# Kernel optimization log

Hardware: AMD Instinct MI355X
Metric: run time of the kernel (lower is better)

Reference implementation:

```python
import jax, jax.numpy as jnp
import numpy as np

B, T, V = 8, 64, 25
IN_DIM = 64
HID = 64
D = 3 * HID // 2          # 96, per-node feature dim
OUT = 128
N = B * T * V * 2         # 25600 nodes
E = N * 16                # 409600 edges
LAYERS = 2
EPS = 1e-5


def prelu(x, a):
    return jnp.where(x >= 0, x, a * x)


def grouped_conv1x1(x, w, b, groups=3):
    # x: [B, C, V, T]; w: [O, C//groups]; b: [O]  (1x1 conv, groups=3)
    Bb, C, Vv, Tt = x.shape
    O = w.shape[0]
    xg = x.reshape(Bb, groups, C // groups, Vv, Tt)
    wg = w.reshape(groups, O // groups, C // groups)
    y = jnp.einsum('bgivt,goi->bgovt', xg, wg).reshape(Bb, O, Vv, Tt)
    return y + b[None, :, None, None]


def layer_norm(x, g, b):
    m = jnp.mean(x, axis=-1, keepdims=True)
    v = jnp.mean((x - m) ** 2, axis=-1, keepdims=True)
    return (x - m) / jnp.sqrt(v + EPS) * g + b


def _forward(h, src, dst, tp_w1, tp_b1, tp_a, tp_w2, tp_b2,
             tm_w1, tm_b1, tm_a, tm_w2, tm_b2,
             ln_g, ln_b, bn_g, bn_b, bn_rm, bn_rv, act_a,
             gW1, gb1, ga, gW2, gb2, t2_w, t2_b):
    # posture / motion streams -> [B, 3*in_dim, V, T]
    hp = jnp.transpose(h[:, :, :, 0, :], (0, 3, 2, 1))
    hm = jnp.transpose(h[:, :, :, 1, :], (0, 3, 2, 1))
    hp = grouped_conv1x1(prelu(grouped_conv1x1(hp, tp_w1, tp_b1), tp_a), tp_w2, tp_b2)
    hm = grouped_conv1x1(prelu(grouped_conv1x1(hm, tm_w1, tm_b1), tm_a), tm_w2, tm_b2)
    hp = jnp.transpose(hp, (0, 3, 2, 1))[:, :, :, None, :]  # [B,T,V,1,D]
    hm = jnp.transpose(hm, (0, 3, 2, 1))[:, :, :, None, :]
    x = jnp.concatenate([hp, hm], axis=3).reshape(-1, D)     # [N, D]
    raw = x
    hs, es = [], []
    for i in range(LAYERS):
        def gate(h2, i=i):
            # edge gate MLP: Linear -> PReLU -> Linear -> Tanh (dropout eval = id)
            return jnp.tanh(prelu(h2 @ gW1[i] + gb1[i], ga[i]) @ gW2[i] + gb2[i])
        e = gate(x[dst] * x[src])                            # [E, 1]
        z = jax.ops.segment_sum(x[src] * e, dst, num_segments=N)
        y = layer_norm(z + x, ln_g[i], ln_b[i])
        y = (y - bn_rm[i]) / jnp.sqrt(bn_rv[i] + EPS) * bn_g[i] + bn_b[i]  # BN eval
        x = prelu(y, act_a[i])
        hs.append(x)
        es.append(gate(x[dst] * x[src]))   # torch calls the layer a 2nd time for e
    hcat = jnp.concatenate([raw] + hs, axis=1)               # [N, 3D]
    out = hcat @ t2_w + t2_b                                 # dropout eval = id
    ee = jnp.concatenate(es, axis=0)                         # [2E, 1]
    return out, ee


def setup_inputs() -> dict:
    key = jax.random.key(0)
    ks = jax.random.split(key, 40)
    def nrm(k, shape, s=0.05):
        return jax.random.normal(k, shape, jnp.float32) * s
    d = {}
    d['h'] = jax.random.normal(ks[0], (B, T, V, 2, 3 * IN_DIM), jnp.float32)
    d['src'] = jax.random.randint(ks[1], (E,), 0, N, jnp.int32)
    d['dst'] = jax.random.randint(ks[2], (E,), 0, N, jnp.int32)
    # t1_posture / t1_motion grouped 1x1 convs
    d['tp_w1'] = nrm(ks[3], (3 * HID, IN_DIM)); d['tp_b1'] = nrm(ks[4], (3 * HID,))
    d['tp_a'] = jnp.full((1,), 0.25, jnp.float32)
    d['tp_w2'] = nrm(ks[5], (D, HID)); d['tp_b2'] = nrm(ks[6], (D,))
    d['tm_w1'] = nrm(ks[7], (3 * HID, IN_DIM)); d['tm_b1'] = nrm(ks[8], (3 * HID,))
    d['tm_a'] = jnp.full((1,), 0.25, jnp.float32)
    d['tm_w2'] = nrm(ks[9], (D, HID)); d['tm_b2'] = nrm(ks[10], (D,))
    # per-layer norms / activations (stacked over LAYERS)
    d['ln_g'] = jnp.ones((LAYERS, D), jnp.float32); d['ln_b'] = jnp.zeros((LAYERS, D), jnp.float32)
    d['bn_g'] = jnp.ones((LAYERS, D), jnp.float32); d['bn_b'] = jnp.zeros((LAYERS, D), jnp.float32)
    d['bn_rm'] = jnp.zeros((LAYERS, D), jnp.float32); d['bn_rv'] = jnp.ones((LAYERS, D), jnp.float32)
    d['act_a'] = jnp.full((LAYERS,), 0.25, jnp.float32)
    # per-layer FALayer gate MLP
    d['gW1'] = nrm(ks[11], (LAYERS, D, D)); d['gb1'] = nrm(ks[12], (LAYERS, D))
    d['ga'] = jnp.full((LAYERS,), 0.25, jnp.float32)
    d['gW2'] = nrm(ks[13], (LAYERS, D, 1)); d['gb2'] = nrm(ks[14], (LAYERS, 1))
    d['t2_w'] = nrm(ks[15], (3 * D, OUT)); d['t2_b'] = nrm(ks[16], (OUT,))
    return d


def reference(h, src, dst, tp_w1, tp_b1, tp_a, tp_w2, tp_b2,
              tm_w1, tm_b1, tm_a, tm_w2, tm_b2,
              ln_g, ln_b, bn_g, bn_b, bn_rm, bn_rv, act_a,
              gW1, gb1, ga, gW2, gb2, t2_w, t2_b):
    return _forward(h, src, dst, tp_w1, tp_b1, tp_a, tp_w2, tp_b2,
                    tm_w1, tm_b1, tm_a, tm_w2, tm_b2,
                    ln_g, ln_b, bn_g, bn_b, bn_rm, bn_rv, act_a,
                    gW1, gb1, ga, gW2, gb2, t2_w, t2_b)
```

## Files before the change

kernel.cpp:

```cpp
#include <hip/hip_runtime.h>

#define N_NODES 25600
#define N_EDGES 409600
#define EPSV 1e-5f

__device__ __forceinline__ unsigned short f2bf(float f) {
    unsigned int x = __float_as_uint(f);
    x += 0x7fffu + ((x >> 16) & 1u);
    return (unsigned short)(x >> 16);
}
__device__ __forceinline__ unsigned int f2bf2(float a, float b) {
#if __has_builtin(__builtin_amdgcn_cvt_pk_bf16_f32)
    auto r = __builtin_amdgcn_cvt_pk_bf16_f32(a, b);
    unsigned int u;
    __builtin_memcpy(&u, &r, 4);
    return u;
#else
    return (unsigned int)f2bf(a) | ((unsigned int)f2bf(b) << 16);
#endif
}

using frag_ab = __attribute__((ext_vector_type(8))) short;
using frag_cd = __attribute__((ext_vector_type(4))) float;
typedef _Float16 f16x8 __attribute__((ext_vector_type(8)));

#define TWST 72
#define THST 200

__global__ __launch_bounds__(256) void transform_mfma(
    const float* __restrict__ h,
    const float* __restrict__ tpw1, const float* __restrict__ tpb1, const float* __restrict__ tpa,
    const float* __restrict__ tpw2, const float* __restrict__ tpb2,
    const float* __restrict__ tmw1, const float* __restrict__ tmb1, const float* __restrict__ tma,
    const float* __restrict__ tmw2, const float* __restrict__ tmb2,
    float* __restrict__ xout, _Float16* __restrict__ xh)
{
    __shared__ alignas(16) unsigned short W1s[192 * TWST];
    __shared__ alignas(16) unsigned short W2s[96 * TWST];
    __shared__ alignas(16) unsigned short hs[64 * THST];
    __shared__ float b1s[192];
    __shared__ float b2s[96];

    const int tid = threadIdx.x;
    const int s = blockIdx.y;
    const float* w1 = s ? tmw1 : tpw1;
    const float* b1 = s ? tmb1 : tpb1;
    const float* w2 = s ? tmw2 : tpw2;
    const float* b2 = s ? tmb2 : tpb2;
    const float alpha = (s ? tma : tpa)[0];

    #pragma unroll
    for (int r = 0; r < 12; r++) {
        int idx4 = r * 256 + tid;
        int o = idx4 >> 4, i4 = (idx4 & 15) * 4;
        const float4 a = *(const float4*)&w1[o * 64 + i4];
        *(uint2*)&W1s[o * TWST + i4] = make_uint2(f2bf2(a.x, a.y), f2bf2(a.z, a.w));
    }
    #pragma unroll
    for (int r = 0; r < 6; r++) {
        int idx4 = r * 256 + tid;
        int o = idx4 >> 4, i4 = (idx4 & 15) * 4;
        const float4 a = *(const float4*)&w2[o * 64 + i4];
        *(uint2*)&W2s[o * TWST + i4] = make_uint2(f2bf2(a.x, a.y), f2bf2(a.z, a.w));
    }
    if (tid < 192) b1s[tid] = b1[tid];
    if (tid < 96) b2s[tid] = b2[tid];
    __syncthreads();

    const int lane = tid & 63;
    const int wv = tid >> 6;
    const int quad = lane >> 4;
    const int lcol = lane & 15;
    const int m0 = wv * 16;
    const int j0 = blockIdx.x * 64;

    #pragma unroll
    for (int r = 0; r < 12; r++) {
        int idx = r * 256 + tid;
        int m = idx / 48, q = idx - m * 48;
        const float4 a = *(const float4*)&h[(2 * (j0 + m) + s) * 192 + q * 4];
        *(uint2*)&hs[m * THST + q * 4] = make_uint2(f2bf2(a.x, a.y), f2bf2(a.z, a.w));
    }
    __syncthreads();

    const int arow = (m0 + lcol) * THST;
    #pragma unroll
    for (int g = 0; g < 3; g++) {
        frag_cd acc[4];
        #pragma unroll
        for (int nt = 0; nt < 4; nt++) acc[nt] = (frag_cd){0.f, 0.f, 0.f, 0.f};
        #pragma unroll
        for (int kt = 0; kt < 2; kt++) {
            const int k0 = kt * 32 + quad * 8;
            frag_ab af = *(const frag_ab*)&hs[arow + g * 64 + k0];
            #pragma unroll
            for (int nt = 0; nt < 4; nt++) {
                frag_ab bf = *(const frag_ab*)&W1s[(g * 64 + nt * 16 + lcol) * TWST + k0];
                acc[nt] = __builtin_amdgcn_mfma_f32_16x16x32_bf16(af, bf, acc[nt], 0, 0, 0);
            }
        }
        #pragma unroll
        for (int nt = 0; nt < 4; nt++) {
            const int o = g * 64 + nt * 16 + lcol;
            const float bv = b1s[o];
            #pragma unroll
            for (int reg = 0; reg < 4; reg++) {
                float u = acc[nt][reg] + bv;
                u = u >= 0.f ? u : alpha * u;
                hs[(m0 + quad * 4 + reg) * THST + o] = f2bf(u);
            }
        }
    }
    #pragma unroll
    for (int g2 = 0; g2 < 3; g2++) {
        frag_cd acc[2];
        acc[0] = (frag_cd){0.f, 0.f, 0.f, 0.f};
        acc[1] = (frag_cd){0.f, 0.f, 0.f, 0.f};
        #pragma unroll
        for (int kt = 0; kt < 2; kt++) {
            const int k0 = kt * 32 + quad * 8;
            frag_ab af = *(const frag_ab*)&hs[arow + g2 * 64 + k0];
            #pragma unroll
            for (int nt = 0; nt < 2; nt++) {
                frag_ab bf = *(const frag_ab*)&W2s[(g2 * 32 + nt * 16 + lcol) * TWST + k0];
                acc[nt] = __builtin_amdgcn_mfma_f32_16x16x32_bf16(af, bf, acc[nt], 0, 0, 0);
            }
        }
        #pragma unroll
        for (int nt = 0; nt < 2; nt++) {
            const int o2 = g2 * 32 + nt * 16 + lcol;
            const float bv = b2s[o2];
            #pragma unroll
            for (int reg = 0; reg < 4; reg++) {
                const int node = 2 * (j0 + m0 + quad * 4 + reg) + s;
                const float v = acc[nt][reg] + bv;
                xout[node * 96 + o2] = v;
                xh[node * 96 + o2] = (_Float16)v;
            }
        }
    }
}

template<bool DUAL>
__global__ __launch_bounds__(256) void gate_kernel(
    const _Float16* __restrict__ xh,
    const int* __restrict__ srcp, const int* __restrict__ dstp,
    const int* __restrict__ mapA,
    const float* __restrict__ gW1, const float* __restrict__ gb1,
    const float* __restrict__ ga,  const float* __restrict__ gW2,
    const float* __restrict__ gb2, int layerA, int layerB,
    float* __restrict__ outA, float* __restrict__ outB)
{
    __shared__ alignas(16) _Float16 W1f[(DUAL ? 2 : 1) * 9216];

    const int tid = threadIdx.x;
    {
        const float* W1p = gW1 + layerA * 9216;
        const float* W1q = gW1 + layerB * 9216;
        for (int fi = tid; fi < 1152; fi += 256) {
            int lc = fi & 15, r = fi >> 4;
            int quad = r & 3, t3 = r >> 2;
            int nt = t3 / 3, kt = t3 - nt * 3;
            int n = nt * 16 + lc, k0 = kt * 32 + quad * 8;
            f16x8 v, w;
            #pragma unroll
            for (int j = 0; j < 8; j++) {
                v[j] = (_Float16)W1p[(k0 + j) * 96 + n];
                if (DUAL) w[j] = (_Float16)W1q[(k0 + j) * 96 + n];
            }
            *(f16x8*)&W1f[fi * 8] = v;
            if (DUAL) *(f16x8*)&W1f[9216 + fi * 8] = w;
        }
    }

    const int lane = tid & 63;
    const int wv   = tid >> 6;
    const int quad = lane >> 4;
    const int lcol = lane & 15;
    const int m0   = wv * 16;
    const int erow = m0 + lcol;
    const int koff = quad * 8;

    float w2A[6], b1A[6], w2B[6], b1B[6];
    #pragma unroll
    for (int nt = 0; nt < 6; nt++) {
        w2A[nt] = gW2[layerA * 96 + nt * 16 + lcol];
        b1A[nt] = gb1[layerA * 96 + nt * 16 + lcol];
        if (DUAL) {
            w2B[nt] = gW2[layerB * 96 + nt * 16 + lcol];
            b1B[nt] = gb1[layerB * 96 + nt * 16 + lcol];
        }
    }
    const float alphaA = ga[layerA];
    const float b2A = gb2[layerA];
    const float alphaB = DUAL ? ga[layerB] : 0.f;
    const float b2B = DUAL ? gb2[layerB] : 0.f;

    int si[4], di[4];
    #pragma unroll
    for (int t = 0; t < 4; t++) {
        const int s = blockIdx.x * 256 + t * 64 + erow;
        si[t] = srcp[s];
        di[t] = dstp[s];
    }
    __syncthreads();

    f16x8 A0, A1, A2, B0, B1, B2;
    {
        const _Float16* rs = xh + si[0] * 96 + koff;
        const _Float16* rd = xh + di[0] * 96 + koff;
        A0 = *(const f16x8*)rs;        B0 = *(const f16x8*)rd;
        A1 = *(const f16x8*)(rs + 32); B1 = *(const f16x8*)(rd + 32);
        A2 = *(const f16x8*)(rs + 64); B2 = *(const f16x8*)(rd + 64);
    }

    #pragma unroll
    for (int t = 0; t < 4; t++) {
        f16x8 p0 = A0 * B0;
        f16x8 p1 = A1 * B1;
        f16x8 p2 = A2 * B2;
        if (t < 3) {
            const _Float16* rs = xh + si[t + 1] * 96 + koff;
            const _Float16* rd = xh + di[t + 1] * 96 + koff;
            A0 = *(const f16x8*)rs;        B0 = *(const f16x8*)rd;
            A1 = *(const f16x8*)(rs + 32); B1 = *(const f16x8*)(rd + 32);
            A2 = *(const f16x8*)(rs + 64); B2 = *(const f16x8*)(rd + 64);
        }

        frag_cd accA[6], accB[6];
        #pragma unroll
        for (int nt = 0; nt < 6; nt++) {
            accA[nt] = (frag_cd){0.f, 0.f, 0.f, 0.f};
            if (DUAL) accB[nt] = (frag_cd){0.f, 0.f, 0.f, 0.f};
        }
        __builtin_amdgcn_s_setprio(1);
        #pragma unroll
        for (int kt = 0; kt < 3; kt++) {
            const f16x8 pk = (kt == 0) ? p0 : (kt == 1 ? p1 : p2);
            #pragma unroll
            for (int nt = 0; nt < 6; nt++) {
                const int f = ((nt * 3 + kt) * 4 + quad) * 16 + lcol;
                f16x8 bfragA = *(const f16x8*)&W1f[f * 8];
                accA[nt] = __builtin_amdgcn_mfma_f32_16x16x32_f16(pk, bfragA, accA[nt], 0, 0, 0);
                if (DUAL) {
                    f16x8 bfragB = *(const f16x8*)&W1f[9216 + f * 8];
                    accB[nt] = __builtin_amdgcn_mfma_f32_16x16x32_f16(pk, bfragB, accB[nt], 0, 0, 0);
                }
            }
        }
        __builtin_amdgcn_s_setprio(0);
        float psA[4] = {0.f, 0.f, 0.f, 0.f};
        float psB[4] = {0.f, 0.f, 0.f, 0.f};
        #pragma unroll
        for (int nt = 0; nt < 6; nt++) {
            #pragma unroll
            for (int reg = 0; reg < 4; reg++) {
                float u = accA[nt][reg] + b1A[nt];
                u = u >= 0.f ? u : alphaA * u;
                psA[reg] += u * w2A[nt];
            }
            if (DUAL) {
                #pragma unroll
                for (int reg = 0; reg < 4; reg++) {
                    float u = accB[nt][reg] + b1B[nt];
                    u = u >= 0.f ? u : alphaB * u;
                    psB[reg] += u * w2B[nt];
                }
            }
        }
        #pragma unroll
        for (int off = 1; off < 4; off <<= 1) {
            #pragma unroll
            for (int reg = 0; reg < 4; reg++) {
                psA[reg] += __shfl_xor(psA[reg], off, 64);
                if (DUAL) psB[reg] += __shfl_xor(psB[reg], off, 64);
            }
        }
        float vA = (lcol & 2) ? ((lcol & 1) ? psA[3] : psA[2])
                              : ((lcol & 1) ? psA[1] : psA[0]);
        vA += __shfl_xor(vA, 4, 64);
        vA += __shfl_xor(vA, 8, 64);
        float vB = 0.f;
        if (DUAL) {
            vB = (lcol & 2) ? ((lcol & 1) ? psB[3] : psB[2])
                            : ((lcol & 1) ? psB[1] : psB[0]);
            vB += __shfl_xor(vB, 4, 64);
            vB += __shfl_xor(vB, 8, 64);
        }
        const float eA = tanhf(vA + b2A);
        const float eB = DUAL ? tanhf(vB + b2B) : 0.f;
        if (lcol < 4) {
            const int slot = blockIdx.x * 256 + t * 64 + m0 + quad * 4 + lcol;
            outA[mapA ? mapA[slot] : slot] = eA;
            if (DUAL) outB[slot] = eB;
        }
    }
}

__global__ __launch_bounds__(256) void count_kernel(
    const int* __restrict__ dst, int* __restrict__ cnt)
{
    int e = blockIdx.x * 256 + threadIdx.x;
    atomicAdd(&cnt[dst[e]], 1);
}

__global__ __launch_bounds__(1024) void scan_kernel(
    const int* __restrict__ cnt, int* __restrict__ off, int* __restrict__ cur)
{
    __shared__ int part[1024];
    const int tid = threadIdx.x;
    const int base = tid * 25;
    int loc[25];
    int s = 0;
    #pragma unroll
    for (int i = 0; i < 25; i++) { loc[i] = s; s += cnt[base + i]; }
    part[tid] = s;
    __syncthreads();
    for (int d = 1; d < 1024; d <<= 1) {
        int t = (tid >= d) ? part[tid - d] : 0;
        __syncthreads();
        part[tid] += t;
        __syncthreads();
    }
    const int basesum = part[tid] - s;
    #pragma unroll
    for (int i = 0; i < 25; i++) {
        int o = basesum + loc[i];
        off[base + i] = o;
        cur[base + i] = o;
    }
    if (tid == 1023) off[N_NODES] = part[1023];
}

__global__ __launch_bounds__(256) void scatter_kernel(
    const int* __restrict__ dst, const int* __restrict__ src,
    int* __restrict__ cur, int* __restrict__ perm,
    int* __restrict__ srcp, int* __restrict__ dstp)
{
    int e = blockIdx.x * 256 + threadIdx.x;
    int d = dst[e];
    int p = atomicAdd(&cur[d], 1);
    perm[p] = e;
    srcp[p] = src[e];
    dstp[p] = d;
}

__global__ __launch_bounds__(256) void prep_t2w(
    const float* __restrict__ t2w, _Float16* __restrict__ t2wf)
{
    int idx = blockIdx.x * 256 + threadIdx.x;
    int j = idx & 7;
    int t = idx >> 3;
    int lc = t & 15;
    int u = t >> 4;
    int c = u % 36, nt = u / 36;
    int o = nt * 16 + lc;
    int ck = c / 12, r = c - ck * 12;
    int kt3 = r >> 2, quad = r & 3;
    int k = ck * 96 + kt3 * 32 + quad * 8 + j;
    t2wf[idx] = (_Float16)t2w[k * 128 + o];
}

__global__ __launch_bounds__(128) void agg_norm_kernel(
    const float* __restrict__ xf, const int* __restrict__ srcp,
    const float* __restrict__ ef,
    const int* __restrict__ off,
    const float* __restrict__ xin,
    const float* __restrict__ lng, const float* __restrict__ lnb,
    const float* __restrict__ bng, const float* __restrict__ bnb,
    const float* __restrict__ bnrm, const float* __restrict__ bnrv,
    const float* __restrict__ acta, int layer,
    float* __restrict__ xout, _Float16* __restrict__ xh)
{
    __shared__ float red[4];
    const int n = blockIdx.x;
    const int tid = threadIdx.x;
    const int wv = tid >> 6;
    const int beg = off[n], end = off[n + 1];
    float v = 0.f;
    if (tid < 96) {
        float v0 = 0.f, v1 = 0.f, v2 = 0.f, v3 = 0.f;
        int j = beg;
        for (; j + 4 <= end; j += 4) {
            v0 += xf[srcp[j] * 96 + tid] * ef[j];
            v1 += xf[srcp[j + 1] * 96 + tid] * ef[j + 1];
            v2 += xf[srcp[j + 2] * 96 + tid] * ef[j + 2];
            v3 += xf[srcp[j + 3] * 96 + tid] * ef[j + 3];
        }
        for (; j < end; j++) {
            v0 += xf[srcp[j] * 96 + tid] * ef[j];
        }
        v = ((v0 + v1) + (v2 + v3)) + xin[n * 96 + tid];
    }
    float r = v;
    #pragma unroll
    for (int o2 = 1; o2 < 64; o2 <<= 1) r += __shfl_xor(r, o2, 64);
    if ((tid & 63) == 0) red[wv] = r;
    __syncthreads();
    const float mean = (red[0] + red[1]) * (1.f / 96.f);
    const float d = (tid < 96) ? (v - mean) : 0.f;
    float r2 = d * d;
    #pragma unroll
    for (int o2 = 1; o2 < 64; o2 <<= 1) r2 += __shfl_xor(r2, o2, 64);
    if ((tid & 63) == 0) red[2 + wv] = r2;
    __syncthreads();
    const float rstd = rsqrtf((red[2] + red[3]) * (1.f / 96.f) + EPSV);
    if (tid < 96) {
        const int c = layer * 96 + tid;
        float y = d * rstd * lng[c] + lnb[c];
        y = (y - bnrm[c]) * rsqrtf(bnrv[c] + EPSV) * bng[c] + bnb[c];
        const float a = acta[layer];
        const float o = y >= 0.f ? y : a * y;
        if (xout) xout[n * 96 + tid] = o;
        xh[n * 96 + tid] = (_Float16)o;
    }
}

__global__ __launch_bounds__(256) void final_mfma(
    const _Float16* __restrict__ xh0, const _Float16* __restrict__ xh1,
    const _Float16* __restrict__ xh2, const _Float16* __restrict__ t2wf,
    const float* __restrict__ t2b, float* __restrict__ out)
{
    const int tid  = threadIdx.x;
    const int lane = tid & 63;
    const int wv   = tid >> 6;
    const int quad = lane >> 4;
    const int lcol = lane & 15;
    const int mrow = blockIdx.x * 64 + wv * 16 + lcol;

    frag_cd acc[8];
    #pragma unroll
    for (int nt = 0; nt < 8; nt++) acc[nt] = (frag_cd){0.f, 0.f, 0.f, 0.f};

    #pragma unroll
    for (int ck = 0; ck < 3; ck++) {
        const _Float16* xc = (ck == 0) ? xh0 : (ck == 1 ? xh1 : xh2);
        const _Float16* ap = xc + mrow * 96 + quad * 8;
        #pragma unroll
        for (int kt3 = 0; kt3 < 3; kt3++) {
            f16x8 afrag = *(const f16x8*)(ap + kt3 * 32);
            const int chunk = 12 * ck + 4 * kt3 + quad;
            #pragma unroll
            for (int nt = 0; nt < 8; nt++) {
                f16x8 bfrag = *(const f16x8*)&t2wf[((nt * 36 + chunk) * 16 + lcol) * 8];
                acc[nt] = __builtin_amdgcn_mfma_f32_16x16x32_f16(afrag, bfrag, acc[nt], 0, 0, 0);
            }
        }
    }
    const int node = blockIdx.x * 64 + wv * 16 + quad * 4;
    #pragma unroll
    for (int nt = 0; nt < 8; nt++) {
        const int o = nt * 16 + lcol;
        const float bias = t2b[o];
        #pragma unroll
        for (int reg = 0; reg < 4; reg++)
            out[(node + reg) * 128 + o] = acc[nt][reg] + bias;
    }
}

extern "C" void kernel_launch(void* const* d_in, const int* in_sizes, int n_in,
                              void* d_out, int out_size, void* d_ws, size_t ws_size,
                              hipStream_t stream)
{
    const float* h    = (const float*)d_in[0];
    const int*   src  = (const int*)d_in[1];
    const int*   dst  = (const int*)d_in[2];
    const float* tpw1 = (const float*)d_in[3];
    const float* tpb1 = (const float*)d_in[4];
    const float* tpa  = (const float*)d_in[5];
    const float* tpw2 = (const float*)d_in[6];
    const float* tpb2 = (const float*)d_in[7];
    const float* tmw1 = (const float*)d_in[8];
    const float* tmb1 = (const float*)d_in[9];
    const float* tma  = (const float*)d_in[10];
    const float* tmw2 = (const float*)d_in[11];
    const float* tmb2 = (const float*)d_in[12];
    const float* lng  = (const float*)d_in[13];
    const float* lnb  = (const float*)d_in[14];
    const float* bng  = (const float*)d_in[15];
    const float* bnb  = (const float*)d_in[16];
    const float* bnrm = (const float*)d_in[17];
    const float* bnrv = (const float*)d_in[18];
    const float* acta = (const float*)d_in[19];
    const float* gW1  = (const float*)d_in[20];
    const float* gb1  = (const float*)d_in[21];
    const float* ga   = (const float*)d_in[22];
    const float* gW2  = (const float*)d_in[23];
    const float* gb2  = (const float*)d_in[24];
    const float* t2w  = (const float*)d_in[25];
    const float* t2b  = (const float*)d_in[26];

    float* ws = (float*)d_ws;
    float* x0 = ws;
    float* x1 = x0 + N_NODES * 96;
    float* eb = x1 + N_NODES * 96;
    _Float16* xh0 = (_Float16*)(eb + N_EDGES);
    _Float16* xh1 = xh0 + N_NODES * 96;
    _Float16* xh2 = xh1 + N_NODES * 96;
    int* cnt  = (int*)(xh2 + N_NODES * 96);
    int* off  = cnt + N_NODES;
    int* cur  = off + N_NODES + 1;
    int* perm = cur + N_NODES;
    int* srcp = perm + N_EDGES;
    int* dstp = srcp + N_EDGES;
    _Float16* t2wf = (_Float16*)cnt;

    float* out = (float*)d_out;
    float* ee  = out + N_NODES * 128;

    hipMemsetAsync(cnt, 0, N_NODES * sizeof(int), stream);
    count_kernel<<<N_EDGES / 256, 256, 0, stream>>>(dst, cnt);
    scan_kernel<<<1, 1024, 0, stream>>>(cnt, off, cur);
    scatter_kernel<<<N_EDGES / 256, 256, 0, stream>>>(dst, src, cur, perm, srcp, dstp);
    prep_t2w<<<144, 256, 0, stream>>>(t2w, t2wf);

    transform_mfma<<<dim3(200, 2), 256, 0, stream>>>(
        h, tpw1, tpb1, tpa, tpw2, tpb2, tmw1, tmb1, tma, tmw2, tmb2, x0, xh0);

    gate_kernel<false><<<1600, 256, 0, stream>>>(xh0, srcp, dstp, nullptr,
        gW1, gb1, ga, gW2, gb2, 0, 0, eb, nullptr);
    agg_norm_kernel<<<N_NODES, 128, 0, stream>>>(x0, srcp, eb, off, x0,
        lng, lnb, bng, bnb, bnrm, bnrv, acta, 0, x1, xh1);

    gate_kernel<true><<<1600, 256, 0, stream>>>(xh1, srcp, dstp, perm,
        gW1, gb1, ga, gW2, gb2, 0, 1, ee, eb);

    agg_norm_kernel<<<N_NODES, 128, 0, stream>>>(x1, srcp, eb, off, x1,
        lng, lnb, bng, bnb, bnrm, bnrv, acta, 1, nullptr, xh2);
    gate_kernel<false><<<1600, 256, 0, stream>>>(xh2, srcp, dstp, perm,
        gW1, gb1, ga, gW2, gb2, 1, 0, ee + N_EDGES, nullptr);

    final_mfma<<<N_NODES / 64, 256, 0, stream>>>(xh0, xh1, xh2, t2wf, t2b, out);
}
```

Baseline: 358.5 us.

## Pre-swizzle gate W1 to fp16 once and fuse last gate with final matmul

A new prep kernel converts and swizzles the gate W1 weights to fp16 MFMA layout once, so each gate block does a plain vectorized copy into shared memory instead of a strided fp32 gather and convert. The last gate launch and the final output matmul are merged into one launch where every fifth block does the final projection, removing a launch and letting the two independent workloads overlap. It adds one small prep launch and reuses the cur buffer for the swizzled weights, which is only safe because scatter has finished with it.

```diff
diff --git a/kernel.cpp b/kernel.cpp
--- a/kernel.cpp
+++ b/kernel.cpp
@@ -142,37 +142,16 @@
 }
 
 template<bool DUAL>
-__global__ __launch_bounds__(256) void gate_kernel(
-    const _Float16* __restrict__ xh,
+__device__ __forceinline__ void gate_body(
+    const _Float16* __restrict__ xh, const _Float16* __restrict__ W1f,
     const int* __restrict__ srcp, const int* __restrict__ dstp,
     const int* __restrict__ mapA,
-    const float* __restrict__ gW1, const float* __restrict__ gb1,
-    const float* __restrict__ ga,  const float* __restrict__ gW2,
-    const float* __restrict__ gb2, int layerA, int layerB,
+    const float* __restrict__ gb1, const float* __restrict__ ga,
+    const float* __restrict__ gW2, const float* __restrict__ gb2,
+    int layerA, int layerB, int gid,
     float* __restrict__ outA, float* __restrict__ outB)
 {
-    __shared__ alignas(16) _Float16 W1f[(DUAL ? 2 : 1) * 9216];
-
-    const int tid = threadIdx.x;
-    {
-        const float* W1p = gW1 + layerA * 9216;
-        const float* W1q = gW1 + layerB * 9216;
-        for (int fi = tid; fi < 1152; fi += 256) {
-            int lc = fi & 15, r = fi >> 4;
-            int quad = r & 3, t3 = r >> 2;
-            int nt = t3 / 3, kt = t3 - nt * 3;
-            int n = nt * 16 + lc, k0 = kt * 32 + quad * 8;
-            f16x8 v, w;
-            #pragma unroll
-            for (int j = 0; j < 8; j++) {
-                v[j] = (_Float16)W1p[(k0 + j) * 96 + n];
-                if (DUAL) w[j] = (_Float16)W1q[(k0 + j) * 96 + n];
-            }
-            *(f16x8*)&W1f[fi * 8] = v;
-            if (DUAL) *(f16x8*)&W1f[9216 + fi * 8] = w;
-        }
-    }
-
+    const int tid  = threadIdx.x;
     const int lane = tid & 63;
     const int wv   = tid >> 6;
     const int quad = lane >> 4;
@@ -199,7 +178,7 @@
     int si[4], di[4];
     #pragma unroll
     for (int t = 0; t < 4; t++) {
-        const int s = blockIdx.x * 256 + t * 64 + erow;
+        const int s = gid * 256 + t * 64 + erow;
         si[t] = srcp[s];
         di[t] = dstp[s];
     }
@@ -290,11 +269,36 @@
         const float eA = tanhf(vA + b2A);
         const float eB = DUAL ? tanhf(vB + b2B) : 0.f;
         if (lcol < 4) {
-            const int slot = blockIdx.x * 256 + t * 64 + m0 + quad * 4 + lcol;
+            const int slot = gid * 256 + t * 64 + m0 + quad * 4 + lcol;
             outA[mapA ? mapA[slot] : slot] = eA;
             if (DUAL) outB[slot] = eB;
         }
     }
+}
+
+template<bool DUAL>
+__global__ __launch_bounds__(256) void gate_kernel(
+    const _Float16* __restrict__ xh,
+    const int* __restrict__ srcp, const int* __restrict__ dstp,
+    const int* __restrict__ mapA,
+    const _Float16* __restrict__ gw1f, const float* __restrict__ gb1,
+    const float* __restrict__ ga,  const float* __restrict__ gW2,
+    const float* __restrict__ gb2, int layerA, int layerB,
+    float* __restrict__ outA, float* __restrict__ outB)
+{
+    __shared__ alignas(16) _Float16 W1f[(DUAL ? 2 : 1) * 9216];
+    const int tid = threadIdx.x;
+    {
+        const uint4* g4 = (const uint4*)(gw1f + layerA * 9216);
+        uint4* l4 = (uint4*)W1f;
+        for (int i = tid; i < 1152; i += 256) l4[i] = g4[i];
+        if (DUAL) {
+            const uint4* h4 = (const uint4*)(gw1f + layerB * 9216);
+            for (int i = tid; i < 1152; i += 256) l4[1152 + i] = h4[i];
+        }
+    }
+    gate_body<DUAL>(xh, W1f, srcp, dstp, mapA, gb1, ga, gW2, gb2,
+                    layerA, layerB, blockIdx.x, outA, outB);
 }
 
 __global__ __launch_bounds__(256) void count_kernel(
@@ -359,6 +363,20 @@
     int kt3 = r >> 2, quad = r & 3;
     int k = ck * 96 + kt3 * 32 + quad * 8 + j;
     t2wf[idx] = (_Float16)t2w[k * 128 + o];
+}
+
+__global__ __launch_bounds__(256) void prep_gw1(
+    const float* __restrict__ gW1, _Float16* __restrict__ gw1f)
+{
+    int idx = blockIdx.x * 256 + threadIdx.x;
+    int layer = idx / 9216;
+    int rem = idx - layer * 9216;
+    int fi = rem >> 3, j = rem & 7;
+    int lc = fi & 15, r = fi >> 4;
+    int quad = r & 3, t3 = r >> 2;
+    int nt = t3 / 3, kt = t3 - nt * 3;
+    int n = nt * 16 + lc, k0 = kt * 32 + quad * 8;
+    gw1f[idx] = (_Float16)gW1[layer * 9216 + (k0 + j) * 96 + n];
 }
 
 __global__ __launch_bounds__(128) void agg_norm_kernel(
@@ -416,17 +434,17 @@
     }
 }
 
-__global__ __launch_bounds__(256) void final_mfma(
+__device__ __forceinline__ void final_body(
     const _Float16* __restrict__ xh0, const _Float16* __restrict__ xh1,
     const _Float16* __restrict__ xh2, const _Float16* __restrict__ t2wf,
-    const float* __restrict__ t2b, float* __restrict__ out)
+    const float* __restrict__ t2b, float* __restrict__ out, int bid)
 {
     const int tid  = threadIdx.x;
     const int lane = tid & 63;
     const int wv   = tid >> 6;
     const int quad = lane >> 4;
     const int lcol = lane & 15;
-    const int mrow = blockIdx.x * 64 + wv * 16 + lcol;
+    const int mrow = bid * 64 + wv * 16 + lcol;
 
     frag_cd acc[8];
     #pragma unroll
@@ -447,7 +465,7 @@
             }
         }
     }
-    const int node = blockIdx.x * 64 + wv * 16 + quad * 4;
+    const int node = bid * 64 + wv * 16 + quad * 4;
     #pragma unroll
     for (int nt = 0; nt < 8; nt++) {
         const int o = nt * 16 + lcol;
@@ -455,6 +473,32 @@
         #pragma unroll
         for (int reg = 0; reg < 4; reg++)
             out[(node + reg) * 128 + o] = acc[nt][reg] + bias;
+    }
+}
+
+__global__ __launch_bounds__(256) void gate_final_kernel(
+    const _Float16* __restrict__ xh0, const _Float16* __restrict__ xh1,
+    const _Float16* __restrict__ xh2,
+    const int* __restrict__ srcp, const int* __restrict__ dstp,
+    const int* __restrict__ perm,
+    const _Float16* __restrict__ gw1f, const float* __restrict__ gb1,
+    const float* __restrict__ ga,  const float* __restrict__ gW2,
+    const float* __restrict__ gb2,
+    const _Float16* __restrict__ t2wf, const float* __restrict__ t2b,
+    float* __restrict__ ee1, float* __restrict__ out)
+{
+    __shared__ alignas(16) _Float16 W1f[9216];
+    const int g = blockIdx.x / 5;
+    const int pos = blockIdx.x - g * 5;
+    if (pos < 4) {
+        const int tid = threadIdx.x;
+        const uint4* g4 = (const uint4*)(gw1f + 9216);
+        uint4* l4 = (uint4*)W1f;
+        for (int i = tid; i < 1152; i += 256) l4[i] = g4[i];
+        gate_body<false>(xh2, W1f, srcp, dstp, perm, gb1, ga, gW2, gb2,
+                         1, 0, g * 4 + pos, ee1, nullptr);
+    } else {
+        final_body(xh0, xh1, xh2, t2wf, t2b, out, g);
     }
 }
 
@@ -504,6 +548,7 @@
     int* srcp = perm + N_EDGES;
     int* dstp = srcp + N_EDGES;
     _Float16* t2wf = (_Float16*)cnt;
+    _Float16* gw1f = (_Float16*)cur;
 
     float* out = (float*)d_out;
     float* ee  = out + N_NODES * 128;
@@ -513,22 +558,22 @@
     scan_kernel<<<1, 1024, 0, stream>>>(cnt, off, cur);
     scatter_kernel<<<N_EDGES / 256, 256, 0, stream>>>(dst, src, cur, perm, srcp, dstp);
     prep_t2w<<<144, 256, 0, stream>>>(t2w, t2wf);
+    prep_gw1<<<72, 256, 0, stream>>>(gW1, gw1f);
 
     transform_mfma<<<dim3(200, 2), 256, 0, stream>>>(
         h, tpw1, tpb1, tpa, tpw2, tpb2, tmw1, tmb1, tma, tmw2, tmb2, x0, xh0);
 
     gate_kernel<false><<<1600, 256, 0, stream>>>(xh0, srcp, dstp, nullptr,
-        gW1, gb1, ga, gW2, gb2, 0, 0, eb, nullptr);
+        gw1f, gb1, ga, gW2, gb2, 0, 0, eb, nullptr);
     agg_norm_kernel<<<N_NODES, 128, 0, stream>>>(x0, srcp, eb, off, x0,
         lng, lnb, bng, bnb, bnrm, bnrv, acta, 0, x1, xh1);
 
     gate_kernel<true><<<1600, 256, 0, stream>>>(xh1, srcp, dstp, perm,
-        gW1, gb1, ga, gW2, gb2, 0, 1, ee, eb);
+        gw1f, gb1, ga, gW2, gb2, 0, 1, ee, eb);
 
     agg_norm_kernel<<<N_NODES, 128, 0, stream>>>(x1, srcp, eb, off, x1,
         lng, lnb, bng, bnb, bnrm, bnrv, acta, 1, nullptr, xh2);
-    gate_kernel<false><<<1600, 256, 0, stream>>>(xh2, srcp, dstp, perm,
-        gW1, gb1, ga, gW2, gb2, 1, 0, ee + N_EDGES, nullptr);
-
-    final_mfma<<<N_NODES / 64, 256, 0, stream>>>(xh0, xh1, xh2, t2wf, t2b, out);
-}
+
+    gate_final_kernel<<<2000, 256, 0, stream>>>(xh0, xh1, xh2, srcp, dstp, perm,
+        gw1f, gb1, ga, gW2, gb2, t2wf, t2b, ee + N_EDGES, out);
+}
```

New measurement: 352.2 us. About the same (-1.8%).
